# Kernel tuning notes

Hardware: AMD Instinct MI355X
Metric: run time of the kernel (lower is better)

## Reference

```python
import jax, jax.numpy as jnp
import numpy as np

B, L, D, H, NL, DFF = 32, 64, 256, 8, 2, 2048
S, I, DSEM, DDENSE, DSPARSE = 16, 16, 128, 128, 128


def layer_norm(x, g, b, eps=1e-5):
    m = x.mean(-1, keepdims=True)
    v = ((x - m) ** 2).mean(-1, keepdims=True)
    return (x - m) / jnp.sqrt(v + eps) * g + b


def encoder_layer(x, ipw, ipb, ow, ob, g1, b1, g2, b2, f1w, f1b, f2w, f2b):
    # PyTorch TransformerEncoderLayer (post-norm, ReLU FFN, dropout inactive).
    b, t, d = x.shape
    dh = d // H
    qkv = x @ ipw.T + ipb  # (b,t,3d)
    q, k, v = jnp.split(qkv, 3, axis=-1)
    split_heads = lambda z: z.reshape(b, t, H, dh).transpose(0, 2, 1, 3)
    q, k, v = split_heads(q), split_heads(k), split_heads(v)
    att = jax.nn.softmax(jnp.einsum('bhqd,bhkd->bhqk', q, k) / np.float32(np.sqrt(dh)), axis=-1)
    o = jnp.einsum('bhqk,bhkd->bhqd', att, v).transpose(0, 2, 1, 3).reshape(b, t, d)
    x = layer_norm(x + o @ ow.T + ob, g1, b1)
    h = jax.nn.relu(x @ f1w.T + f1b) @ f2w.T + f2b
    return layer_norm(x + h, g2, b2)


def setup_inputs() -> dict:
    key = jax.random.key(0)
    ks = jax.random.split(key, 16)
    sc = np.float32(0.02)
    return dict(
        dense=jax.random.normal(ks[0], (B, L, DDENSE), jnp.float32),
        sparse=jax.random.normal(ks[1], (B, L, DSPARSE), jnp.float32),
        W_feat=jax.random.normal(ks[2], (DDENSE + DSPARSE, D), jnp.float32) * sc,
        b_feat=jnp.zeros((D,), jnp.float32),
        in_proj_w=jax.random.normal(ks[3], (NL, 3 * D, D), jnp.float32) * sc,
        in_proj_b=jnp.zeros((NL, 3 * D), jnp.float32),
        out_w=jax.random.normal(ks[4], (NL, D, D), jnp.float32) * sc,
        out_b=jnp.zeros((NL, D), jnp.float32),
        ln1_g=jnp.ones((NL, D), jnp.float32), ln1_b=jnp.zeros((NL, D), jnp.float32),
        ln2_g=jnp.ones((NL, D), jnp.float32), ln2_b=jnp.zeros((NL, D), jnp.float32),
        ff1_w=jax.random.normal(ks[5], (NL, DFF, D), jnp.float32) * sc,
        ff1_b=jnp.zeros((NL, DFF), jnp.float32),
        ff2_w=jax.random.normal(ks[6], (NL, D, DFF), jnp.float32) * sc,
        ff2_b=jnp.zeros((NL, D), jnp.float32),
        w_act=jax.random.normal(ks[7], (D, 1), jnp.float32) * sc,
        w_route_ws=jax.random.normal(ks[8], (L, S, D), jnp.float32) * sc,
        w_pose_ws=jax.random.normal(ks[9], (L, S, D, D), jnp.float32) * sc,
        w_route_si=jax.random.normal(ks[10], (S, I, D), jnp.float32) * sc,
        w_pose_si=jax.random.normal(ks[11], (S, I, D, D), jnp.float32) * sc,
        cls_w=jax.random.normal(ks[12], (DSEM, 2 * D), jnp.float32) * sc,
        cls_b=jnp.zeros((DSEM,), jnp.float32),
        inorm_g=jnp.ones((DSEM,), jnp.float32),
        inorm_b=jnp.zeros((DSEM,), jnp.float32),
    )


def reference(dense, sparse, W_feat, b_feat, in_proj_w, in_proj_b, out_w, out_b,
              ln1_g, ln1_b, ln2_g, ln2_b, ff1_w, ff1_b, ff2_w, ff2_b,
              w_act, w_route_ws, w_pose_ws, w_route_si, w_pose_si,
              cls_w, cls_b, inorm_g, inorm_b):
    # TokenFeaturizer: concat(dense, sparse) -> Linear -> (b,L,d)
    tok = jnp.concatenate([dense, sparse], axis=-1) @ W_feat + b_feat
    cls = tok.sum(axis=1, keepdims=True)  # einsum 'bld->bd' CLS token
    x = jnp.concatenate([tok, cls], axis=1)  # (b, L+1, d)
    for i in range(in_proj_w.shape[0]):
        x = encoder_layer(x, in_proj_w[i], in_proj_b[i], out_w[i], out_b[i],
                          ln1_g[i], ln1_b[i], ln2_g[i], ln2_b[i],
                          ff1_w[i], ff1_b[i], ff2_w[i], ff2_b[i])
    words, cls_tok = x[:, :L], x[:, L]  # (b,L,d), (b,d)

    # --- route words -> slots ('weighted_sig') ---
    a_words = jax.nn.sigmoid((words @ w_act)[..., 0])  # (b,L)
    c_ws = jax.nn.softmax(jnp.einsum('lsd,bld->bls', w_route_ws, words), axis=-1)
    a_num = jnp.einsum('bls,bl->bs', c_ws, a_words)
    a_slots = a_num / a_words.sum(axis=1, keepdims=True)
    u_hat = jnp.einsum('lsij,blj->blsi', w_pose_ws, words)  # (b,L,S,d)
    u_num = jnp.einsum('bls,bl,blsi->bsi', c_ws, a_words, u_hat)
    u_slots = u_num / a_num[..., None]  # (b,S,d)

    # --- route slots -> intents ---
    c_si = jax.nn.softmax(jnp.einsum('sid,bsd->bsi', w_route_si, u_slots), axis=-1)
    an = jnp.einsum('bsi,bs->bi', c_si, a_slots)
    a_intents = an / (a_slots.sum(axis=1, keepdims=True) + 1e-8)
    u_hat_i = jnp.einsum('sijk,bsk->bsik', w_pose_si, u_slots)  # (b,S,I,d)
    un = jnp.einsum('bsi,bs,bsik->bik', c_si, a_slots, u_hat_i)
    u_intents = un / (an[..., None] + 1e-8)  # (b,I,d)

    # argmax over intents, gather winning pose
    idx = jnp.argmax(a_intents, axis=-1)  # (b,)
    poses = u_intents[jnp.arange(u_intents.shape[0]), idx]  # (b,d)
    intents = jnp.concatenate([cls_tok, poses], axis=-1) @ cls_w.T + cls_b
    intents = layer_norm(intents, inorm_g, inorm_b)
    return (c_ws, intents)
```

## Files before the change

### kernel.cpp

```cpp
#include <hip/hip_runtime.h>
#include <hip/hip_bf16.h>
#include <math.h>

#define B_ 32
#define L_ 64
#define D_ 256
#define H_ 8
#define T_ 65
#define NT_ (B_*T_)
#define DFF_ 2048
#define S_ 16
#define I_ 16
#define DSEM_ 128

typedef __attribute__((ext_vector_type(8))) short bf16x8;
typedef __attribute__((ext_vector_type(4))) float f32x4;

typedef __attribute__((address_space(1))) const void gbl_void;
typedef __attribute__((address_space(3))) void lds_void;
#define GLOAD16(g, l) __builtin_amdgcn_global_load_lds((gbl_void*)(g), (lds_void*)(l), 16, 0, 0)

__device__ inline unsigned short f2bu(float f) {
  union { float f; unsigned u; } a; a.f = f;
  unsigned r = a.u + 0x7FFF + ((a.u >> 16) & 1);
  return (unsigned short)(r >> 16);
}
__device__ inline float b2f(unsigned short u) {
  union { unsigned u; float f; } a; a.u = ((unsigned)u) << 16;
  return a.f;
}

__device__ inline float wave_reduce_sum(float v) {
#pragma unroll
  for (int m = 32; m >= 1; m >>= 1) v += __shfl_xor(v, m, 64);
  return v;
}

__device__ inline float block_reduce_sum_256(float v, float* sred) {
  v = wave_reduce_sum(v);
  int tid = threadIdx.x;
  if ((tid & 63) == 0) sred[tid >> 6] = v;
  __syncthreads();
  float r = sred[0] + sred[1] + sred[2] + sred[3];
  __syncthreads();
  return r;
}

__global__ void concat_bf_kernel(const float* __restrict__ dense, const float* __restrict__ sparse,
                                 unsigned short* __restrict__ cat) {
  int idx = blockIdx.x * 256 + threadIdx.x;
  int r = idx >> 8, c = idx & 255;
  float v = (c < 128) ? dense[r * 128 + c] : sparse[r * 128 + (c - 128)];
  cat[idx] = f2bu(v);
}

__global__ void conv_all_kernel(const float* __restrict__ ipw, const float* __restrict__ ow,
                                const float* __restrict__ f1w, const float* __restrict__ f2w,
                                unsigned short* __restrict__ ipwB, unsigned short* __restrict__ owB,
                                unsigned short* __restrict__ f1wB, unsigned short* __restrict__ f2wB) {
  int i = blockIdx.x * 256 + threadIdx.x;
  const float* src; unsigned short* dst; int off;
  if (i < 98304)       { src = ipw; dst = ipwB; off = i; }
  else if (i < 131072) { src = ow;  dst = owB;  off = i - 98304; }
  else if (i < 393216) { src = f1w; dst = f1wB; off = i - 131072; }
  else                 { src = f2w; dst = f2wB; off = i - 393216; }
  float4 v = ((const float4*)src)[off];
  short4 o;
  o.x = (short)f2bu(v.x); o.y = (short)f2bu(v.y);
  o.z = (short)f2bu(v.z); o.w = (short)f2bu(v.w);
  ((short4*)dst)[off] = o;
}

__global__ __launch_bounds__(256) void transpose_f2b_kernel(const float* __restrict__ in,
                                                            unsigned short* __restrict__ out) {
  __shared__ float t[64][65];
  int blk = blockIdx.x;
  int k0 = (blk & 3) * 64, n0 = (blk >> 2) * 64;
  int wid = threadIdx.x >> 6, lane = threadIdx.x & 63;
#pragma unroll
  for (int p = 0; p < 16; ++p) {
    int kk = p * 4 + wid;
    t[kk][lane] = in[(size_t)(k0 + kk) * 256 + n0 + lane];
  }
  __syncthreads();
#pragma unroll
  for (int p = 0; p < 16; ++p) {
    int nn = p * 4 + wid;
    out[(size_t)(n0 + nn) * 256 + k0 + lane] = f2bu(t[lane][nn]);
  }
}

template <int ACT, int OUT_BF16, int NFRAG>
__global__ __launch_bounds__(256) void gemm_bf2_kernel(const unsigned short* __restrict__ A,
                                                       const unsigned short* __restrict__ W,
                                                       const float* __restrict__ bias,
                                                       float* __restrict__ Cf, unsigned short* __restrict__ Cb,
                                                       int M, int N, int K) {
  __shared__ __align__(16) unsigned short As[2][32 * 64];
  __shared__ __align__(16) unsigned short Bs[2][NFRAG * 64 * 64];
  int tid = threadIdx.x, wid = tid >> 6, lane = tid & 63;
  int row0 = blockIdx.y * 32, col0 = blockIdx.x * (64 * NFRAG);
  int lr = lane >> 3;
  int sc = ((lane & 7) ^ (lr & 7)) << 3;
  const unsigned short* Asrc = A + (size_t)(row0 + wid * 8 + lr) * K + sc;
  const unsigned short* Bsrc[2 * NFRAG];
#pragma unroll
  for (int p = 0; p < 2 * NFRAG; ++p)
    Bsrc[p] = W + (size_t)(col0 + wid * 16 * NFRAG + p * 8 + lr) * K + sc;
  unsigned short* AsW = &As[0][0] + wid * (8 * 64);
  unsigned short* BsW = &Bs[0][0] + wid * (16 * NFRAG * 64);

  f32x4 acc[2][NFRAG];
#pragma unroll
  for (int i = 0; i < 2; ++i)
#pragma unroll
    for (int j = 0; j < NFRAG; ++j) acc[i][j] = (f32x4){0.f, 0.f, 0.f, 0.f};

  GLOAD16(Asrc, AsW);
#pragma unroll
  for (int p = 0; p < 2 * NFRAG; ++p) GLOAD16(Bsrc[p], BsW + p * (8 * 64));

  int nk = K >> 6, cur = 0;
  int kg = lane >> 4, l15 = lane & 15;
  for (int kt = 0; kt < nk; ++kt) {
    __syncthreads();
    if (kt + 1 < nk) {
      int k0 = (kt + 1) << 6;
      GLOAD16(Asrc + k0, AsW + (cur ^ 1) * (32 * 64));
#pragma unroll
      for (int p = 0; p < 2 * NFRAG; ++p)
        GLOAD16(Bsrc[p] + k0, BsW + (cur ^ 1) * (NFRAG * 64 * 64) + p * (8 * 64));
    }
    const unsigned short* Ab = &As[cur][0];
    const unsigned short* Bb = &Bs[cur][0];
#pragma unroll
    for (int kk = 0; kk < 2; ++kk) {
      int cc = kk * 4 + kg;
      bf16x8 bfr[NFRAG];
#pragma unroll
      for (int fn = 0; fn < NFRAG; ++fn) {
        int rn = wid * 16 * NFRAG + fn * 16 + l15;
        bfr[fn] = *(const bf16x8*)&Bb[rn * 64 + ((cc ^ (rn & 7)) << 3)];
      }
#pragma unroll
      for (int fm = 0; fm < 2; ++fm) {
        int rm = fm * 16 + l15;
        bf16x8 afr = *(const bf16x8*)&Ab[rm * 64 + ((cc ^ (rm & 7)) << 3)];
#pragma unroll
        for (int fn = 0; fn < NFRAG; ++fn)
          acc[fm][fn] = __builtin_amdgcn_mfma_f32_16x16x32_bf16(afr, bfr[fn], acc[fm][fn], 0, 0, 0);
      }
    }
    cur ^= 1;
  }
#pragma unroll
  for (int fm = 0; fm < 2; ++fm) {
#pragma unroll
    for (int fn = 0; fn < NFRAG; ++fn) {
      int col = col0 + wid * 16 * NFRAG + fn * 16 + l15;
      float bi = bias[col];
      int rbase = row0 + fm * 16 + ((lane >> 4) << 2);
#pragma unroll
      for (int r = 0; r < 4; ++r) {
        int grow = rbase + r;
        float v = acc[fm][fn][r] + bi;
        if (ACT == 1) v = fmaxf(v, 0.f);
        if (OUT_BF16) Cb[(size_t)grow * N + col] = f2bu(v);
        else          Cf[(size_t)grow * N + col] = v;
      }
    }
  }
}

__global__ __launch_bounds__(256) void gemm_ln_kernel(const unsigned short* __restrict__ A,
                                                      const unsigned short* __restrict__ W,
                                                      const float* __restrict__ bias,
                                                      const float* __restrict__ gw, const float* __restrict__ gb,
                                                      float* X, unsigned short* __restrict__ xbf,
                                                      int K) {
  __shared__ __align__(16) unsigned short As[2][32 * 64];
  __shared__ __align__(16) unsigned short Bs[2][4 * 64 * 64];
  __shared__ float sred[4][32], sredq[4][32];
  int tid = threadIdx.x, wid = tid >> 6, lane = tid & 63;
  int row0 = blockIdx.y * 32;
  int lr = lane >> 3;
  int sc = ((lane & 7) ^ (lr & 7)) << 3;
  const unsigned short* Asrc = A + (size_t)(row0 + wid * 8 + lr) * K + sc;
  const unsigned short* Bsrc[8];
#pragma unroll
  for (int p = 0; p < 8; ++p)
    Bsrc[p] = W + (size_t)(wid * 64 + p * 8 + lr) * K + sc;
  unsigned short* AsW = &As[0][0] + wid * (8 * 64);
  unsigned short* BsW = &Bs[0][0] + wid * (64 * 64);

  f32x4 acc[2][4];
#pragma unroll
  for (int i = 0; i < 2; ++i)
#pragma unroll
    for (int j = 0; j < 4; ++j) acc[i][j] = (f32x4){0.f, 0.f, 0.f, 0.f};

  GLOAD16(Asrc, AsW);
#pragma unroll
  for (int p = 0; p < 8; ++p) GLOAD16(Bsrc[p], BsW + p * (8 * 64));

  int nk = K >> 6, cur = 0;
  int kg = lane >> 4, l15 = lane & 15;
  for (int kt = 0; kt < nk; ++kt) {
    __syncthreads();
    if (kt + 1 < nk) {
      int k0 = (kt + 1) << 6;
      GLOAD16(Asrc + k0, AsW + (cur ^ 1) * (32 * 64));
#pragma unroll
      for (int p = 0; p < 8; ++p)
        GLOAD16(Bsrc[p] + k0, BsW + (cur ^ 1) * (4 * 64 * 64) + p * (8 * 64));
    }
    const unsigned short* Ab = &As[cur][0];
    const unsigned short* Bb = &Bs[cur][0];
#pragma unroll
    for (int kk = 0; kk < 2; ++kk) {
      int cc = kk * 4 + kg;
      bf16x8 bfr[4];
#pragma unroll
      for (int fn = 0; fn < 4; ++fn) {
        int rn = wid * 64 + fn * 16 + l15;
        bfr[fn] = *(const bf16x8*)&Bb[rn * 64 + ((cc ^ (rn & 7)) << 3)];
      }
#pragma unroll
      for (int fm = 0; fm < 2; ++fm) {
        int rm = fm * 16 + l15;
        bf16x8 afr = *(const bf16x8*)&Ab[rm * 64 + ((cc ^ (rm & 7)) << 3)];
#pragma unroll
        for (int fn = 0; fn < 4; ++fn)
          acc[fm][fn] = __builtin_amdgcn_mfma_f32_16x16x32_bf16(afr, bfr[fn], acc[fm][fn], 0, 0, 0);
      }
    }
    cur ^= 1;
  }
  int g = lane >> 4;
  float v[2][4][4];
  float rs[2][4], rq[2][4];
#pragma unroll
  for (int fm = 0; fm < 2; ++fm)
#pragma unroll
    for (int r = 0; r < 4; ++r) { rs[fm][r] = 0.f; rq[fm][r] = 0.f; }
#pragma unroll
  for (int fm = 0; fm < 2; ++fm) {
    int grow0 = row0 + fm * 16 + g * 4;
#pragma unroll
    for (int fn = 0; fn < 4; ++fn) {
      int col = wid * 64 + fn * 16 + l15;
      float bi = bias[col];
#pragma unroll
      for (int r = 0; r < 4; ++r) {
        float val = acc[fm][fn][r] + bi + X[(size_t)(grow0 + r) * 256 + col];
        v[fm][fn][r] = val;
        rs[fm][r] += val;
        rq[fm][r] += val * val;
      }
    }
  }
#pragma unroll
  for (int m = 1; m <= 8; m <<= 1) {
#pragma unroll
    for (int fm = 0; fm < 2; ++fm)
#pragma unroll
      for (int r = 0; r < 4; ++r) {
        rs[fm][r] += __shfl_xor(rs[fm][r], m, 64);
        rq[fm][r] += __shfl_xor(rq[fm][r], m, 64);
      }
  }
  if (l15 == 0) {
#pragma unroll
    for (int fm = 0; fm < 2; ++fm)
#pragma unroll
      for (int r = 0; r < 4; ++r) {
        int row = fm * 16 + g * 4 + r;
        sred[wid][row] = rs[fm][r];
        sredq[wid][row] = rq[fm][r];
      }
  }
  __syncthreads();
#pragma unroll
  for (int fm = 0; fm < 2; ++fm) {
#pragma unroll
    for (int r = 0; r < 4; ++r) {
      int row = fm * 16 + g * 4 + r;
      float tsum = sred[0][row] + sred[1][row] + sred[2][row] + sred[3][row];
      float tsq = sredq[0][row] + sredq[1][row] + sredq[2][row] + sredq[3][row];
      float mean = tsum * (1.f / 256.f);
      float var = tsq * (1.f / 256.f) - mean * mean;
      float rstd = 1.f / sqrtf(var + 1e-5f);
      int grow = row0 + row;
#pragma unroll
      for (int fn = 0; fn < 4; ++fn) {
        int col = wid * 64 + fn * 16 + l15;
        float o = (v[fm][fn][r] - mean) * rstd * gw[col] + gb[col];
        X[(size_t)grow * 256 + col] = o;
        xbf[(size_t)grow * 256 + col] = f2bu(o);
      }
    }
  }
}

__global__ void build_x_kernel(const float* __restrict__ tok, float* __restrict__ x,
                               unsigned short* __restrict__ xbf) {
  int b = blockIdx.x, d = threadIdx.x;
  float s = 0.f;
  for (int l = 0; l < L_; ++l) {
    float v = tok[((size_t)(b * L_ + l)) * D_ + d];
    size_t o = ((size_t)(b * T_ + l)) * D_ + d;
    x[o] = v; xbf[o] = f2bu(v);
    s += v;
  }
  size_t o = ((size_t)(b * T_ + L_)) * D_ + d;
  x[o] = s; xbf[o] = f2bu(s);
}

__global__ __launch_bounds__(256) void attn_kernel(const unsigned short* __restrict__ qkv,
                                                   unsigned short* __restrict__ attn_out) {
  int bh = blockIdx.x;
  int b = bh >> 3, h = bh & 7;
  __shared__ float Q[T_][32], K[T_][32], V[T_][32];
  __shared__ float Sc[T_][T_ + 1];
  int tid = threadIdx.x;
  for (int idx = tid; idx < T_ * 32; idx += 256) {
    int t = idx >> 5, d = idx & 31;
    const unsigned short* base = qkv + ((size_t)(b * T_ + t)) * 768 + h * 32 + d;
    Q[t][d] = b2f(base[0]);
    K[t][d] = b2f(base[256]);
    V[t][d] = b2f(base[512]);
  }
  __syncthreads();
  for (int idx = tid; idx < T_ * T_; idx += 256) {
    int qi = idx / T_, ki = idx % T_;
    float s = 0.f;
#pragma unroll
    for (int d = 0; d < 32; ++d) s += Q[qi][d] * K[ki][d];
    Sc[qi][ki] = s * 0.17677669529663687f;
  }
  __syncthreads();
  {
    int q = tid & 3;
    for (int row = tid >> 2; row < T_; row += 64) {
      float mx = -1e30f;
      for (int k = q; k < T_; k += 4) mx = fmaxf(mx, Sc[row][k]);
      mx = fmaxf(mx, __shfl_xor(mx, 1, 64));
      mx = fmaxf(mx, __shfl_xor(mx, 2, 64));
      float sum = 0.f;
      for (int k = q; k < T_; k += 4) { float e = expf(Sc[row][k] - mx); Sc[row][k] = e; sum += e; }
      sum += __shfl_xor(sum, 1, 64);
      sum += __shfl_xor(sum, 2, 64);
      float inv = 1.f / sum;
      for (int k = q; k < T_; k += 4) Sc[row][k] *= inv;
    }
  }
  __syncthreads();
  for (int idx = tid; idx < T_ * 32; idx += 256) {
    int t = idx >> 5, d = idx & 31;
    float acc = 0.f;
    for (int k = 0; k < T_; ++k) acc += Sc[t][k] * V[k][d];
    attn_out[((size_t)(b * T_ + t)) * D_ + h * 32 + d] = f2bu(acc);
  }
}

__global__ __launch_bounds__(256) void cws_kernel(const float* __restrict__ x, const float* __restrict__ w_route,
                                                  const float* __restrict__ w_act, float* __restrict__ c_ws_out,
                                                  float* __restrict__ a_words) {
  int bl = blockIdx.x;
  int b = bl >> 6, l = bl & 63;
  __shared__ float word[256];
  __shared__ float logits[16];
  __shared__ float sred[4];
  int t = threadIdx.x;
  word[t] = x[((size_t)(b * T_ + l)) * D_ + t];
  __syncthreads();
  float pa = word[t] * w_act[t];
  float asum = block_reduce_sum_256(pa, sred);
  if (t == 0) a_words[b * 64 + l] = 1.f / (1.f + expf(-asum));
  int s = t >> 4, j0 = t & 15;
  float p = 0.f;
  for (int j = j0; j < 256; j += 16) p += w_route[((size_t)(l * 16 + s)) * 256 + j] * word[j];
#pragma unroll
  for (int m = 8; m >= 1; m >>= 1) p += __shfl_xor(p, m, 64);
  if (j0 == 0) logits[s] = p;
  __syncthreads();
  if (t < 16) {
    float mx = -1e30f;
#pragma unroll
    for (int k = 0; k < 16; ++k) mx = fmaxf(mx, logits[k]);
    float sum = 0.f;
#pragma unroll
    for (int k = 0; k < 16; ++k) sum += expf(logits[k] - mx);
    c_ws_out[(size_t)bl * 16 + t] = expf(logits[t] - mx) / sum;
  }
}

__global__ __launch_bounds__(64) void slot_agg_kernel(const float* __restrict__ c_ws, const float* __restrict__ a_words,
                                                      float* __restrict__ a_num, float* __restrict__ a_slots,
                                                      float* __restrict__ asl_sum) {
  int b = blockIdx.x, lane = threadIdx.x;
  float aw = a_words[b * 64 + lane];
  float asum = wave_reduce_sum(aw);
  float inv = 1.f / asum;
  float ssum = 0.f;
  for (int s = 0; s < 16; ++s) {
    float p = c_ws[((size_t)(b * 64 + lane)) * 16 + s] * aw;
    float r = wave_reduce_sum(p);
    if (lane == 0) {
      a_num[b * 16 + s] = r;
      a_slots[b * 16 + s] = r * inv;
      ssum += r * inv;
    }
  }
  if (lane == 0) asl_sum[b] = ssum;
}

__global__ __launch_bounds__(256, 4) void pose_ws2_kernel(const unsigned short* __restrict__ xbf,
                                                          const float* __restrict__ P,
                                                          const float* __restrict__ c_ws,
                                                          const float* __restrict__ a_words,
                                                          float* __restrict__ partial) {
  int lg = blockIdx.x >> 4, s = blockIdx.x & 15;
  __shared__ __align__(16) unsigned short Bs[32 * 256];
  int tid = threadIdx.x, wid = tid >> 6, lane = tid & 63;
  int kg = lane >> 4;
  f32x4 acc[4][2];
#pragma unroll
  for (int i = 0; i < 4; ++i)
#pragma unroll
    for (int j = 0; j < 2; ++j) acc[i][j] = (f32x4){0.f, 0.f, 0.f, 0.f};

#pragma unroll
  for (int li = 0; li < 2; ++li) {
    int l = lg + li * 32;
    __syncthreads();
    {
      int b = tid >> 3, c0 = (tid & 7) * 4;
      float w = c_ws[((size_t)(b * 64 + l)) * 16 + s] * a_words[b * 64 + l];
      const unsigned short* src = xbf + ((size_t)(b * T_ + l)) * D_;
#pragma unroll
      for (int j = 0; j < 4; ++j) {
        int c = c0 + j;
        union { float4 f4; unsigned short u[8]; } in, out;
        in.f4 = *(const float4*)(src + c * 8);
#pragma unroll
        for (int e = 0; e < 8; ++e) out.u[e] = f2bu(w * b2f(in.u[e]));
        *(float4*)&Bs[b * 256 + ((c ^ (b & 7)) << 3)] = out.f4;
      }
    }
    __syncthreads();
    const float* Pbase = P + (((size_t)(l * 16 + s)) << 16);
#pragma unroll
    for (int k0 = 0; k0 < 256; k0 += 64) {
#pragma unroll
      for (int kk = 0; kk < 2; ++kk) {
        int cc = (k0 >> 3) + kk * 4 + kg;
        bf16x8 bfr[2];
#pragma unroll
        for (int fn = 0; fn < 2; ++fn) {
          int rb = fn * 16 + (lane & 15);
          bfr[fn] = *(const bf16x8*)&Bs[rb * 256 + ((cc ^ (rb & 7)) << 3)];
        }
        int kbase = k0 + kk * 32 + kg * 8;
#pragma unroll
        for (int fm = 0; fm < 4; ++fm) {
          int row = wid * 64 + fm * 16 + (lane & 15);
          const float* src = Pbase + (size_t)row * 256 + kbase;
          float4 v0 = *(const float4*)src;
          float4 v1 = *(const float4*)(src + 4);
          union { bf16x8 b8; unsigned short u[8]; } pk;
          pk.u[0] = f2bu(v0.x); pk.u[1] = f2bu(v0.y); pk.u[2] = f2bu(v0.z); pk.u[3] = f2bu(v0.w);
          pk.u[4] = f2bu(v1.x); pk.u[5] = f2bu(v1.y); pk.u[6] = f2bu(v1.z); pk.u[7] = f2bu(v1.w);
          acc[fm][0] = __builtin_amdgcn_mfma_f32_16x16x32_bf16(pk.b8, bfr[0], acc[fm][0], 0, 0, 0);
          acc[fm][1] = __builtin_amdgcn_mfma_f32_16x16x32_bf16(pk.b8, bfr[1], acc[fm][1], 0, 0, 0);
        }
      }
    }
  }
  float* pout = partial + ((size_t)(lg * 16 + s)) * 8192;
#pragma unroll
  for (int fm = 0; fm < 4; ++fm) {
#pragma unroll
    for (int fn = 0; fn < 2; ++fn) {
      int b = fn * 16 + (lane & 15);
      int i0 = wid * 64 + fm * 16 + ((lane >> 4) << 2);
#pragma unroll
      for (int r = 0; r < 4; ++r)
        pout[(i0 + r) * 32 + b] = acc[fm][fn][r];
    }
  }
}

__global__ __launch_bounds__(256) void reduce_uslots_kernel(const float* __restrict__ partial,
                                                            const float* __restrict__ a_num,
                                                            float* __restrict__ u_slots) {
  int s = blockIdx.x >> 5, ic = blockIdx.x & 31;
  int t = threadIdx.x;
  int i = ic * 8 + (t >> 5), b = t & 31;
  size_t off = (size_t)s * 8192 + i * 32 + b;
  float a0 = 0.f, a1 = 0.f, a2 = 0.f, a3 = 0.f;
#pragma unroll
  for (int lg = 0; lg < 32; lg += 4) {
    a0 += partial[((size_t)(lg + 0) * 16) * 8192 + off];
    a1 += partial[((size_t)(lg + 1) * 16) * 8192 + off];
    a2 += partial[((size_t)(lg + 2) * 16) * 8192 + off];
    a3 += partial[((size_t)(lg + 3) * 16) * 8192 + off];
  }
  u_slots[((size_t)(b * 16 + s)) * 256 + i] = (a0 + a1 + a2 + a3) / a_num[b * 16 + s];
}

__global__ __launch_bounds__(256) void csi_kernel(const float* __restrict__ u_slots, const float* __restrict__ w_route_si,
                                                  float* __restrict__ c_si) {
  int bs = blockIdx.x;
  int s = bs & 15;
  __shared__ float row[256];
  __shared__ float logits[16];
  int t = threadIdx.x;
  row[t] = u_slots[(size_t)bs * 256 + t];
  __syncthreads();
  int i = t >> 4, j0 = t & 15;
  float p = 0.f;
  for (int j = j0; j < 256; j += 16) p += w_route_si[((size_t)(s * 16 + i)) * 256 + j] * row[j];
#pragma unroll
  for (int m = 8; m >= 1; m >>= 1) p += __shfl_xor(p, m, 64);
  if (j0 == 0) logits[i] = p;
  __syncthreads();
  if (t < 16) {
    float mx = -1e30f;
#pragma unroll
    for (int k = 0; k < 16; ++k) mx = fmaxf(mx, logits[k]);
    float sum = 0.f;
#pragma unroll
    for (int k = 0; k < 16; ++k) sum += expf(logits[k] - mx);
    c_si[(size_t)bs * 16 + t] = expf(logits[t] - mx) / sum;
  }
}

__global__ __launch_bounds__(64) void intent_agg_kernel(const float* __restrict__ c_si, const float* __restrict__ a_slots,
                                                        const float* __restrict__ asl_sum, float* __restrict__ an,
                                                        int* __restrict__ idxb) {
  int b = blockIdx.x, lane = threadIdx.x;
  __shared__ float an_s[16];
  if (lane < 16) {
    float acc = 0.f;
    for (int s = 0; s < 16; ++s) acc += c_si[((size_t)(b * 16 + s)) * 16 + lane] * a_slots[b * 16 + s];
    an[b * 16 + lane] = acc;
    an_s[lane] = acc;
  }
  __syncthreads();
  if (lane == 0) {
    float inv = 1.f / (asl_sum[b] + 1e-8f);
    int best = 0;
    float bv = an_s[0] * inv;
    for (int k = 1; k < 16; ++k) {
      float v = an_s[k] * inv;
      if (v > bv) { bv = v; best = k; }
    }
    idxb[b] = best;
  }
}

__global__ void pose_si_partial_kernel(const float* __restrict__ P, float* __restrict__ R4) {
  int si = blockIdx.x >> 2, jc = blockIdx.x & 3;
  int k = threadIdx.x;
  const float* base = P + (size_t)si * 65536 + (size_t)jc * 64 * 256 + k;
  float a0 = 0.f, a1 = 0.f, a2 = 0.f, a3 = 0.f;
#pragma unroll
  for (int j = 0; j < 64; j += 4) {
    a0 += base[(j + 0) * 256];
    a1 += base[(j + 1) * 256];
    a2 += base[(j + 2) * 256];
    a3 += base[(j + 3) * 256];
  }
  R4[(size_t)jc * 65536 + si * 256 + k] = a0 + a1 + a2 + a3;
}

__global__ void r4sum_kernel(const float* __restrict__ R4, float* __restrict__ R) {
  int idx = blockIdx.x * 256 + threadIdx.x;
  R[idx] = R4[idx] + R4[65536 + idx] + R4[131072 + idx] + R4[196608 + idx];
}

__global__ void un32_kernel(const float* __restrict__ c_si, const float* __restrict__ a_slots,
                            const float* __restrict__ R, const float* __restrict__ u_slots,
                            const float* __restrict__ an, const int* __restrict__ idxb,
                            float* __restrict__ u_pose) {
  int b = blockIdx.x, k = threadIdx.x;
  int i = idxb[b];
  float acc = 0.f;
  for (int s = 0; s < 16; ++s) {
    float w = c_si[((size_t)(b * 16 + s)) * 16 + i] * a_slots[b * 16 + s];
    acc += w * R[((size_t)(s * 16 + i)) * 256 + k] * u_slots[((size_t)(b * 16 + s)) * 256 + k];
  }
  u_pose[(size_t)b * 256 + k] = acc / (an[b * 16 + i] + 1e-8f);
}

__global__ __launch_bounds__(128) void final_kernel(const float* __restrict__ x, const float* __restrict__ u_pose,
                                                    const float* __restrict__ cls_w,
                                                    const float* __restrict__ cls_b, const float* __restrict__ g,
                                                    const float* __restrict__ bb, float* __restrict__ out) {
  int b = blockIdx.x, m = threadIdx.x;
  __shared__ float row[512];
  __shared__ float sred[2];
  for (int d = m; d < 256; d += 128) {
    row[d] = x[((size_t)(b * T_ + L_)) * D_ + d];
    row[256 + d] = u_pose[(size_t)b * 256 + d];
  }
  __syncthreads();
  float acc = cls_b[m];
  for (int j = 0; j < 512; ++j) acc += cls_w[(size_t)m * 512 + j] * row[j];
  float v = wave_reduce_sum(acc);
  if ((m & 63) == 0) sred[m >> 6] = v;
  __syncthreads();
  float mean = (sred[0] + sred[1]) * (1.f / 128.f);
  __syncthreads();
  float dv = acc - mean;
  float v2 = wave_reduce_sum(dv * dv);
  if ((m & 63) == 0) sred[m >> 6] = v2;
  __syncthreads();
  float var = (sred[0] + sred[1]) * (1.f / 128.f);
  out[(size_t)b * 128 + m] = dv * (1.f / sqrtf(var + 1e-5f)) * g[m] + bb[m];
}

extern "C" void kernel_launch(void* const* d_in, const int* in_sizes, int n_in,
                              void* d_out, int out_size, void* d_ws, size_t ws_size,
                              hipStream_t stream) {
  (void)in_sizes; (void)n_in; (void)out_size; (void)ws_size;
  const float* dense      = (const float*)d_in[0];
  const float* sparse     = (const float*)d_in[1];
  const float* W_feat     = (const float*)d_in[2];
  const float* b_feat     = (const float*)d_in[3];
  const float* in_proj_w  = (const float*)d_in[4];
  const float* in_proj_b  = (const float*)d_in[5];
  const float* out_w      = (const float*)d_in[6];
  const float* out_b      = (const float*)d_in[7];
  const float* ln1_g      = (const float*)d_in[8];
  const float* ln1_b      = (const float*)d_in[9];
  const float* ln2_g      = (const float*)d_in[10];
  const float* ln2_b      = (const float*)d_in[11];
  const float* ff1_w      = (const float*)d_in[12];
  const float* ff1_b      = (const float*)d_in[13];
  const float* ff2_w      = (const float*)d_in[14];
  const float* ff2_b      = (const float*)d_in[15];
  const float* w_act      = (const float*)d_in[16];
  const float* w_route_ws = (const float*)d_in[17];
  const float* w_pose_ws  = (const float*)d_in[18];
  const float* w_route_si = (const float*)d_in[19];
  const float* w_pose_si  = (const float*)d_in[20];
  const float* cls_w      = (const float*)d_in[21];
  const float* cls_b      = (const float*)d_in[22];
  const float* inorm_g    = (const float*)d_in[23];
  const float* inorm_b    = (const float*)d_in[24];

  float* ws = (float*)d_ws;
  float* X       = ws;
  float* PROJ    = X + 532480;
  float* a_words = PROJ + 532480;
  float* a_num   = a_words + 2048;
  float* a_slots = a_num + 512;
  float* asl_sum = a_slots + 512;
  float* u_slots = asl_sum + 32;
  float* c_si    = u_slots + 131072;
  float* an      = c_si + 8192;
  float* Rbuf    = an + 512;
  float* u_pose  = Rbuf + 65536;
  float* R4      = u_pose + 8192;
  int*   idxb    = (int*)(R4 + 262144);

  unsigned short* bfb   = (unsigned short*)(R4 + 262144 + 32);
  unsigned short* Xbf   = bfb;
  unsigned short* QKVbf = Xbf + 532480;
  unsigned short* HAR   = QKVbf + 1597440;
  unsigned short* CATbf = HAR;
  unsigned short* ATTNbf= HAR + 2097152;
  unsigned short* wfeatT= HAR + 4259840;
  unsigned short* ipwB  = wfeatT + 65536;
  unsigned short* owB   = ipwB + 393216;
  unsigned short* f1wB  = owB + 131072;
  unsigned short* f2wB  = f1wB + 1048576;
  float* partial = (float*)QKVbf;

  float* c_ws_out    = (float*)d_out;
  float* intents_out = (float*)d_out + 32768;

  concat_bf_kernel<<<2048, 256, 0, stream>>>(dense, sparse, CATbf);
  transpose_f2b_kernel<<<16, 256, 0, stream>>>(W_feat, wfeatT);
  conv_all_kernel<<<2560, 256, 0, stream>>>(in_proj_w, out_w, ff1_w, ff2_w, ipwB, owB, f1wB, f2wB);

  gemm_bf2_kernel<0, 0, 1><<<dim3(4, 64), 256, 0, stream>>>(CATbf, wfeatT, b_feat, PROJ, nullptr, 2048, 256, 256);
  build_x_kernel<<<32, 256, 0, stream>>>(PROJ, X, Xbf);

  for (int layer = 0; layer < 2; ++layer) {
    const unsigned short* ipw = ipwB + (size_t)layer * 196608;
    const unsigned short* ow  = owB + (size_t)layer * 65536;
    const unsigned short* f1w = f1wB + (size_t)layer * 524288;
    const unsigned short* f2w = f2wB + (size_t)layer * 524288;
    const float* ipb = in_proj_b + (size_t)layer * 768;
    const float* ob  = out_b + (size_t)layer * 256;
    const float* g1  = ln1_g + (size_t)layer * 256;
    const float* b1  = ln1_b + (size_t)layer * 256;
    const float* g2  = ln2_g + (size_t)layer * 256;
    const float* b2  = ln2_b + (size_t)layer * 256;
    const float* f1b = ff1_b + (size_t)layer * DFF_;
    const float* f2b = ff2_b + (size_t)layer * 256;

    gemm_bf2_kernel<0, 1, 2><<<dim3(6, 65), 256, 0, stream>>>(Xbf, ipw, ipb, nullptr, QKVbf, NT_, 768, 256);
    attn_kernel<<<B_ * H_, 256, 0, stream>>>(QKVbf, ATTNbf);
    gemm_ln_kernel<<<dim3(1, 65), 256, 0, stream>>>(ATTNbf, ow, ob, g1, b1, X, Xbf, 256);
    gemm_bf2_kernel<1, 1, 2><<<dim3(16, 65), 256, 0, stream>>>(Xbf, f1w, f1b, nullptr, HAR, NT_, DFF_, 256);
    gemm_ln_kernel<<<dim3(1, 65), 256, 0, stream>>>(HAR, f2w, f2b, g2, b2, X, Xbf, 2048);
  }

  cws_kernel<<<2048, 256, 0, stream>>>(X, w_route_ws, w_act, c_ws_out, a_words);
  slot_agg_kernel<<<32, 64, 0, stream>>>(c_ws_out, a_words, a_num, a_slots, asl_sum);
  pose_ws2_kernel<<<512, 256, 0, stream>>>(Xbf, w_pose_ws, c_ws_out, a_words, partial);
  reduce_uslots_kernel<<<512, 256, 0, stream>>>(partial, a_num, u_slots);
  pose_si_partial_kernel<<<1024, 256, 0, stream>>>(w_pose_si, R4);
  r4sum_kernel<<<256, 256, 0, stream>>>(R4, Rbuf);
  csi_kernel<<<512, 256, 0, stream>>>(u_slots, w_route_si, c_si);
  intent_agg_kernel<<<32, 64, 0, stream>>>(c_si, a_slots, asl_sum, an, idxb);
  un32_kernel<<<32, 256, 0, stream>>>(c_si, a_slots, Rbuf, u_slots, an, idxb, u_pose);
  final_kernel<<<32, 128, 0, stream>>>(X, u_pose, cls_w, cls_b, inorm_g, inorm_b, intents_out);
}
```

Measured before the change: 304.2 us.

## Fuse conversion kernels, split pose_ws over intent halves, merge intent tail kernels

Three prologue conversion kernels (concat, W_feat transpose, weight bf16 conversion) become one launch dispatched by block index. The pose_ws kernel now splits the output rows into two halves, so twice as many blocks each do half the MFMA work. The r4sum, intent_agg and un32 kernels are merged into one kernel that computes an, the argmax and the pose sum, reading R4 directly. This cuts launch count and raises parallelism in pose_ws, but the Bs staging in pose_ws is now done twice per (l,s), and the argmax drops the positive scale factor.

New measurement: 299.3 us. About the same (-1.6%).

```diff
diff --git a/kernel.cpp b/kernel.cpp
--- a/kernel.cpp
+++ b/kernel.cpp
@@ -46,47 +46,43 @@
   return r;
 }
 
-__global__ void concat_bf_kernel(const float* __restrict__ dense, const float* __restrict__ sparse,
-                                 unsigned short* __restrict__ cat) {
-  int idx = blockIdx.x * 256 + threadIdx.x;
-  int r = idx >> 8, c = idx & 255;
-  float v = (c < 128) ? dense[r * 128 + c] : sparse[r * 128 + (c - 128)];
-  cat[idx] = f2bu(v);
-}
-
-__global__ void conv_all_kernel(const float* __restrict__ ipw, const float* __restrict__ ow,
-                                const float* __restrict__ f1w, const float* __restrict__ f2w,
-                                unsigned short* __restrict__ ipwB, unsigned short* __restrict__ owB,
-                                unsigned short* __restrict__ f1wB, unsigned short* __restrict__ f2wB) {
-  int i = blockIdx.x * 256 + threadIdx.x;
-  const float* src; unsigned short* dst; int off;
-  if (i < 98304)       { src = ipw; dst = ipwB; off = i; }
-  else if (i < 131072) { src = ow;  dst = owB;  off = i - 98304; }
-  else if (i < 393216) { src = f1w; dst = f1wB; off = i - 131072; }
-  else                 { src = f2w; dst = f2wB; off = i - 393216; }
-  float4 v = ((const float4*)src)[off];
-  short4 o;
-  o.x = (short)f2bu(v.x); o.y = (short)f2bu(v.y);
-  o.z = (short)f2bu(v.z); o.w = (short)f2bu(v.w);
-  ((short4*)dst)[off] = o;
-}
-
-__global__ __launch_bounds__(256) void transpose_f2b_kernel(const float* __restrict__ in,
-                                                            unsigned short* __restrict__ out) {
-  __shared__ float t[64][65];
-  int blk = blockIdx.x;
-  int k0 = (blk & 3) * 64, n0 = (blk >> 2) * 64;
-  int wid = threadIdx.x >> 6, lane = threadIdx.x & 63;
-#pragma unroll
-  for (int p = 0; p < 16; ++p) {
-    int kk = p * 4 + wid;
-    t[kk][lane] = in[(size_t)(k0 + kk) * 256 + n0 + lane];
-  }
-  __syncthreads();
-#pragma unroll
-  for (int p = 0; p < 16; ++p) {
-    int nn = p * 4 + wid;
-    out[(size_t)(n0 + nn) * 256 + k0 + lane] = f2bu(t[lane][nn]);
+__global__ __launch_bounds__(256) void conv_fused_kernel(
+    const float* __restrict__ dense, const float* __restrict__ sparse, unsigned short* __restrict__ cat,
+    const float* __restrict__ wfeat, unsigned short* __restrict__ wfeatT,
+    const float* __restrict__ ipw, const float* __restrict__ ow,
+    const float* __restrict__ f1w, const float* __restrict__ f2w,
+    unsigned short* __restrict__ ipwB, unsigned short* __restrict__ owB,
+    unsigned short* __restrict__ f1wB, unsigned short* __restrict__ f2wB) {
+  __shared__ float tb[64][65];
+  int bid = blockIdx.x, tid = threadIdx.x;
+  if (bid < 2048) {
+    int idx = bid * 256 + tid;
+    int r = idx >> 8, c = idx & 255;
+    float v = (c < 128) ? dense[r * 128 + c] : sparse[r * 128 + (c - 128)];
+    cat[idx] = f2bu(v);
+  } else if (bid < 2064) {
+    int blk = bid - 2048;
+    int k0 = (blk & 3) * 64, n0 = (blk >> 2) * 64;
+    int wid = tid >> 6, lane = tid & 63;
+#pragma unroll
+    for (int p = 0; p < 16; ++p)
+      tb[p * 4 + wid][lane] = wfeat[(size_t)(k0 + p * 4 + wid) * 256 + n0 + lane];
+    __syncthreads();
+#pragma unroll
+    for (int p = 0; p < 16; ++p)
+      wfeatT[(size_t)(n0 + p * 4 + wid) * 256 + k0 + lane] = f2bu(tb[lane][p * 4 + wid]);
+  } else {
+    int i = (bid - 2064) * 256 + tid;
+    const float* src; unsigned short* dst; int off;
+    if (i < 98304)       { src = ipw; dst = ipwB; off = i; }
+    else if (i < 131072) { src = ow;  dst = owB;  off = i - 98304; }
+    else if (i < 393216) { src = f1w; dst = f1wB; off = i - 131072; }
+    else                 { src = f2w; dst = f2wB; off = i - 393216; }
+    float4 v = ((const float4*)src)[off];
+    short4 o;
+    o.x = (short)f2bu(v.x); o.y = (short)f2bu(v.y);
+    o.z = (short)f2bu(v.z); o.w = (short)f2bu(v.w);
+    ((short4*)dst)[off] = o;
   }
 }
 
@@ -415,18 +411,20 @@
   if (lane == 0) asl_sum[b] = ssum;
 }
 
-__global__ __launch_bounds__(256, 4) void pose_ws2_kernel(const unsigned short* __restrict__ xbf,
+__global__ __launch_bounds__(256, 4) void pose_ws3_kernel(const unsigned short* __restrict__ xbf,
                                                           const float* __restrict__ P,
                                                           const float* __restrict__ c_ws,
                                                           const float* __restrict__ a_words,
                                                           float* __restrict__ partial) {
-  int lg = blockIdx.x >> 4, s = blockIdx.x & 15;
+  int bid = blockIdx.x;
+  int ih = bid & 1, s = (bid >> 1) & 15, lg = bid >> 5;
+  int iBase = ih * 128;
   __shared__ __align__(16) unsigned short Bs[32 * 256];
   int tid = threadIdx.x, wid = tid >> 6, lane = tid & 63;
-  int kg = lane >> 4;
-  f32x4 acc[4][2];
-#pragma unroll
-  for (int i = 0; i < 4; ++i)
+  int kg = lane >> 4, l15 = lane & 15;
+  f32x4 acc[2][2];
+#pragma unroll
+  for (int i = 0; i < 2; ++i)
 #pragma unroll
     for (int j = 0; j < 2; ++j) acc[i][j] = (f32x4){0.f, 0.f, 0.f, 0.f};
 
@@ -458,13 +456,13 @@
         bf16x8 bfr[2];
 #pragma unroll
         for (int fn = 0; fn < 2; ++fn) {
-          int rb = fn * 16 + (lane & 15);
+          int rb = fn * 16 + l15;
           bfr[fn] = *(const bf16x8*)&Bs[rb * 256 + ((cc ^ (rb & 7)) << 3)];
         }
         int kbase = k0 + kk * 32 + kg * 8;
 #pragma unroll
-        for (int fm = 0; fm < 4; ++fm) {
-          int row = wid * 64 + fm * 16 + (lane & 15);
+        for (int fm = 0; fm < 2; ++fm) {
+          int row = iBase + wid * 32 + fm * 16 + l15;
           const float* src = Pbase + (size_t)row * 256 + kbase;
           float4 v0 = *(const float4*)src;
           float4 v1 = *(const float4*)(src + 4);
@@ -479,11 +477,11 @@
   }
   float* pout = partial + ((size_t)(lg * 16 + s)) * 8192;
 #pragma unroll
-  for (int fm = 0; fm < 4; ++fm) {
+  for (int fm = 0; fm < 2; ++fm) {
 #pragma unroll
     for (int fn = 0; fn < 2; ++fn) {
-      int b = fn * 16 + (lane & 15);
-      int i0 = wid * 64 + fm * 16 + ((lane >> 4) << 2);
+      int b = fn * 16 + l15;
+      int i0 = iBase + wid * 32 + fm * 16 + (kg << 2);
 #pragma unroll
       for (int r = 0; r < 4; ++r)
         pout[(i0 + r) * 32 + b] = acc[fm][fn][r];
@@ -536,30 +534,6 @@
   }
 }
 
-__global__ __launch_bounds__(64) void intent_agg_kernel(const float* __restrict__ c_si, const float* __restrict__ a_slots,
-                                                        const float* __restrict__ asl_sum, float* __restrict__ an,
-                                                        int* __restrict__ idxb) {
-  int b = blockIdx.x, lane = threadIdx.x;
-  __shared__ float an_s[16];
-  if (lane < 16) {
-    float acc = 0.f;
-    for (int s = 0; s < 16; ++s) acc += c_si[((size_t)(b * 16 + s)) * 16 + lane] * a_slots[b * 16 + s];
-    an[b * 16 + lane] = acc;
-    an_s[lane] = acc;
-  }
-  __syncthreads();
-  if (lane == 0) {
-    float inv = 1.f / (asl_sum[b] + 1e-8f);
-    int best = 0;
-    float bv = an_s[0] * inv;
-    for (int k = 1; k < 16; ++k) {
-      float v = an_s[k] * inv;
-      if (v > bv) { bv = v; best = k; }
-    }
-    idxb[b] = best;
-  }
-}
-
 __global__ void pose_si_partial_kernel(const float* __restrict__ P, float* __restrict__ R4) {
   int si = blockIdx.x >> 2, jc = blockIdx.x & 3;
   int k = threadIdx.x;
@@ -575,23 +549,48 @@
   R4[(size_t)jc * 65536 + si * 256 + k] = a0 + a1 + a2 + a3;
 }
 
-__global__ void r4sum_kernel(const float* __restrict__ R4, float* __restrict__ R) {
-  int idx = blockIdx.x * 256 + threadIdx.x;
-  R[idx] = R4[idx] + R4[65536 + idx] + R4[131072 + idx] + R4[196608 + idx];
-}
-
-__global__ void un32_kernel(const float* __restrict__ c_si, const float* __restrict__ a_slots,
-                            const float* __restrict__ R, const float* __restrict__ u_slots,
-                            const float* __restrict__ an, const int* __restrict__ idxb,
-                            float* __restrict__ u_pose) {
-  int b = blockIdx.x, k = threadIdx.x;
-  int i = idxb[b];
+__global__ __launch_bounds__(256) void un_merged_kernel(const float* __restrict__ c_si,
+                                                        const float* __restrict__ a_slots,
+                                                        const float* __restrict__ R4,
+                                                        const float* __restrict__ u_slots,
+                                                        float* __restrict__ u_pose) {
+  int b = blockIdx.x, t = threadIdx.x;
+  __shared__ float csi_s[256];
+  __shared__ float asl_s[16];
+  __shared__ float an_s[16];
+  __shared__ float w_s[16];
+  __shared__ float an_star;
+  __shared__ int istar_s;
+  csi_s[t] = c_si[(size_t)b * 256 + t];
+  if (t < 16) asl_s[t] = a_slots[b * 16 + t];
+  __syncthreads();
+  if (t < 16) {
+    float acc = 0.f;
+#pragma unroll
+    for (int s = 0; s < 16; ++s) acc += csi_s[s * 16 + t] * asl_s[s];
+    an_s[t] = acc;
+  }
+  __syncthreads();
+  if (t == 0) {
+    int best = 0;
+    float bv = an_s[0];
+    for (int k = 1; k < 16; ++k)
+      if (an_s[k] > bv) { bv = an_s[k]; best = k; }
+    istar_s = best;
+    an_star = bv;
+  }
+  __syncthreads();
+  int istar = istar_s;
+  if (t < 16) w_s[t] = csi_s[t * 16 + istar] * asl_s[t];
+  __syncthreads();
   float acc = 0.f;
+#pragma unroll
   for (int s = 0; s < 16; ++s) {
-    float w = c_si[((size_t)(b * 16 + s)) * 16 + i] * a_slots[b * 16 + s];
-    acc += w * R[((size_t)(s * 16 + i)) * 256 + k] * u_slots[((size_t)(b * 16 + s)) * 256 + k];
-  }
-  u_pose[(size_t)b * 256 + k] = acc / (an[b * 16 + i] + 1e-8f);
+    size_t ro = ((size_t)(s * 16 + istar)) * 256 + t;
+    float r = R4[ro] + R4[65536 + ro] + R4[131072 + ro] + R4[196608 + ro];
+    acc += w_s[s] * r * u_slots[((size_t)(b * 16 + s)) * 256 + t];
+  }
+  u_pose[(size_t)b * 256 + t] = acc / (an_star + 1e-8f);
 }
 
 __global__ __launch_bounds__(128) void final_kernel(const float* __restrict__ x, const float* __restrict__ u_pose,
@@ -660,13 +659,10 @@
   float* asl_sum = a_slots + 512;
   float* u_slots = asl_sum + 32;
   float* c_si    = u_slots + 131072;
-  float* an      = c_si + 8192;
-  float* Rbuf    = an + 512;
-  float* u_pose  = Rbuf + 65536;
+  float* u_pose  = c_si + 8192;
   float* R4      = u_pose + 8192;
-  int*   idxb    = (int*)(R4 + 262144);
-
-  unsigned short* bfb   = (unsigned short*)(R4 + 262144 + 32);
+
+  unsigned short* bfb   = (unsigned short*)(R4 + 262144);
   unsigned short* Xbf   = bfb;
   unsigned short* QKVbf = Xbf + 532480;
   unsigned short* HAR   = QKVbf + 1597440;
@@ -682,9 +678,9 @@
   float* c_ws_out    = (float*)d_out;
   float* intents_out = (float*)d_out + 32768;
 
-  concat_bf_kernel<<<2048, 256, 0, stream>>>(dense, sparse, CATbf);
-  transpose_f2b_kernel<<<16, 256, 0, stream>>>(W_feat, wfeatT);
-  conv_all_kernel<<<2560, 256, 0, stream>>>(in_proj_w, out_w, ff1_w, ff2_w, ipwB, owB, f1wB, f2wB);
+  conv_fused_kernel<<<4624, 256, 0, stream>>>(dense, sparse, CATbf, W_feat, wfeatT,
+                                              in_proj_w, out_w, ff1_w, ff2_w,
+                                              ipwB, owB, f1wB, f2wB);
 
   gemm_bf2_kernel<0, 0, 1><<<dim3(4, 64), 256, 0, stream>>>(CATbf, wfeatT, b_feat, PROJ, nullptr, 2048, 256, 256);
   build_x_kernel<<<32, 256, 0, stream>>>(PROJ, X, Xbf);
@@ -712,12 +708,10 @@
 
   cws_kernel<<<2048, 256, 0, stream>>>(X, w_route_ws, w_act, c_ws_out, a_words);
   slot_agg_kernel<<<32, 64, 0, stream>>>(c_ws_out, a_words, a_num, a_slots, asl_sum);
-  pose_ws2_kernel<<<512, 256, 0, stream>>>(Xbf, w_pose_ws, c_ws_out, a_words, partial);
+  pose_ws3_kernel<<<1024, 256, 0, stream>>>(Xbf, w_pose_ws, c_ws_out, a_words, partial);
   reduce_uslots_kernel<<<512, 256, 0, stream>>>(partial, a_num, u_slots);
   pose_si_partial_kernel<<<1024, 256, 0, stream>>>(w_pose_si, R4);
-  r4sum_kernel<<<256, 256, 0, stream>>>(R4, Rbuf);
   csi_kernel<<<512, 256, 0, stream>>>(u_slots, w_route_si, c_si);
-  intent_agg_kernel<<<32, 64, 0, stream>>>(c_si, a_slots, asl_sum, an, idxb);
-  un32_kernel<<<32, 256, 0, stream>>>(c_si, a_slots, Rbuf, u_slots, an, idxb, u_pose);
+  un_merged_kernel<<<32, 256, 0, stream>>>(c_si, a_slots, R4, u_slots, u_pose);
   final_kernel<<<32, 128, 0, stream>>>(X, u_pose, cls_w, cls_b, inorm_g, inorm_b, intents_out);
 }
```
